# Kernel optimization log

Hardware: AMD Instinct MI355X
Metric: run time of the kernel (lower is better)

The kernel has to match this reference:

```python
import jax, jax.numpy as jnp
import numpy as np

N_NODES = 50000
N_EDGES = 600000
BAG = 16
VOCAB = 10000
EMB = 128
HID = 128
N_CLASSES = 10
N_GRAPHS = 512
PAD_IDX = 1


def setup_inputs() -> dict:
    key = jax.random.key(0)
    ks = jax.random.split(key, 12)
    x_tokens = jax.random.randint(ks[0], (N_NODES, BAG), 0, VOCAB)
    src = jax.random.randint(ks[1], (N_EDGES,), 0, N_NODES)
    dst = jax.random.randint(ks[2], (N_EDGES,), 0, N_NODES)
    edge_index = jnp.stack([src, dst])
    batch = jnp.sort(jax.random.randint(ks[3], (N_NODES,), 0, N_GRAPHS))
    # rows 0,1 are zero in the original (weights[2:] filled from pretrained vectors)
    emb_table = (jax.random.normal(ks[4], (VOCAB, EMB)) * 0.02).at[:2].set(0.0)
    s = 1.0 / np.sqrt(EMB)
    w1_l = jax.random.normal(ks[5], (HID, EMB)) * s
    b1 = jnp.zeros((HID,), jnp.float32)
    w1_r = jax.random.normal(ks[6], (HID, EMB)) * s
    w2_l = jax.random.normal(ks[7], (HID, HID)) * s
    b2 = jnp.zeros((HID,), jnp.float32)
    w2_r = jax.random.normal(ks[8], (HID, HID)) * s
    w_out = jax.random.normal(ks[9], (N_CLASSES, HID)) * s
    b_out = jnp.zeros((N_CLASSES,), jnp.float32)
    return {"x_tokens": x_tokens, "edge_index": edge_index, "batch": batch,
            "emb_table": emb_table, "w1_l": w1_l, "b1": b1, "w1_r": w1_r,
            "w2_l": w2_l, "b2": b2, "w2_r": w2_r, "w_out": w_out, "b_out": b_out}


def _embedding_bag_mean(tokens, table):
    # nn.EmbeddingBag mode='mean' with padding_idx: padding tokens excluded from mean
    emb = table[tokens]                                  # [N, BAG, D]
    mask = (tokens != PAD_IDX)[..., None].astype(table.dtype)
    total = jnp.sum(emb * mask, axis=1)                  # [N, D]
    cnt = jnp.clip(jnp.sum(mask, axis=1), 1.0)           # [N, 1]
    return total / cnt


def _sage_conv(x, src, dst, w_l, b_l, w_r):
    # PyG SAGEConv: lin_l(mean_{j in N(i)} x_j) + lin_r(x_i); lin_r has no bias
    n = x.shape[0]
    msg_sum = jax.ops.segment_sum(x[src], dst, num_segments=n)           # [N, D]
    deg = jax.ops.segment_sum(jnp.ones((src.shape[0], 1), x.dtype), dst,
                              num_segments=n)                             # [N, 1]
    aggr = msg_sum / jnp.clip(deg, 1.0)
    return aggr @ w_l.T + b_l + x @ w_r.T


def reference(x_tokens, edge_index, batch, emb_table, w1_l, b1, w1_r,
              w2_l, b2, w2_r, w_out, b_out):
    src, dst = edge_index[0], edge_index[1]
    x = _embedding_bag_mean(x_tokens, emb_table)                 # [N, EMB]
    x = jax.nn.relu(_sage_conv(x, src, dst, w1_l, b1, w1_r))     # [N, HID]
    x = jax.nn.relu(_sage_conv(x, src, dst, w2_l, b2, w2_r))     # [N, HID]
    # global_mean_pool over graph ids
    g_sum = jax.ops.segment_sum(x, batch, num_segments=N_GRAPHS)
    g_cnt = jax.ops.segment_sum(jnp.ones((x.shape[0], 1), x.dtype), batch,
                                num_segments=N_GRAPHS)
    g = g_sum / jnp.clip(g_cnt, 1.0)                             # [G, HID]
    return g @ w_out.T + b_out                                   # [G, C]
```

## Files before the change

kernel.cpp:

```cpp
#include <hip/hip_runtime.h>
#include <hip/hip_bf16.h>

#define NN 50000
#define NE 600000
#define BAG 16
#define EMB 128
#define HID 128
#define NC 10
#define NG 512
#define PAD_IDX 1
#define VOCAB 10000
#define SLOTS 64
#define TPAIRS (VOCAB * EMB / 2)
#define WPAIRS (4 * HID * EMB / 2)
#define NE8 (NE / 8)
#define SC8BLK ((NE8 + 255) / 256)
#define EMVB (NN / 16)
#define NTILES ((NN + 127) / 128)

typedef __attribute__((ext_vector_type(8))) short v8s;
typedef __attribute__((ext_vector_type(4))) float v4f;

__device__ __forceinline__ float bflo(unsigned u) { return __uint_as_float(u << 16); }
__device__ __forceinline__ float bfhi(unsigned u) { return __uint_as_float(u & 0xffff0000u); }
__device__ __forceinline__ unsigned short f2bf(float f) {
    unsigned u = __float_as_uint(f);
    return (unsigned short)((u + 0x7fffu + ((u >> 16) & 1u)) >> 16);
}
__device__ __forceinline__ void acc8(float* a, v8s v) {
    unsigned* u = (unsigned*)&v;
#pragma unroll
    for (int j = 0; j < 4; j++) {
        a[2 * j] += bflo(u[j]);
        a[2 * j + 1] += bfhi(u[j]);
    }
}

__global__ void k_conv(const float* __restrict__ t, unsigned short* __restrict__ tb,
                       const float* __restrict__ w1l, const float* __restrict__ w1r,
                       const float* __restrict__ w2l, const float* __restrict__ w2r,
                       unsigned short* __restrict__ wbf, int* __restrict__ cnt,
                       float* __restrict__ gsum, float* __restrict__ gcnt) {
    int i = blockIdx.x * blockDim.x + threadIdx.x;
    if (i < NN) cnt[i] = 0;
    if (i < NG * HID) gsum[i] = 0.f;
    if (i < NG) gcnt[i] = 0.f;
    if (i < TPAIRS) {
        float2 v = *(const float2*)(t + (size_t)i * 2);
        unsigned lo = f2bf(v.x), hi = f2bf(v.y);
        *(unsigned*)(tb + (size_t)i * 2) = lo | (hi << 16);
    } else if (i < TPAIRS + WPAIRS) {
        int j = i - TPAIRS;
        int k = j * 2;
        int arr = k >> 14;
        int o = k & 16383;
        const float* w = (arr == 0) ? w1l : (arr == 1) ? w1r : (arr == 2) ? w2l : w2r;
        float2 v = *(const float2*)(w + o);
        unsigned lo = f2bf(v.x), hi = f2bf(v.y);
        *(unsigned*)(wbf + k) = lo | (hi << 16);
    }
}

__global__ __launch_bounds__(256) void k_scatem(const int* __restrict__ src,
                                                const int* __restrict__ dst,
                                                int* __restrict__ cnt,
                                                int* __restrict__ slots,
                                                const int* __restrict__ tokens,
                                                const unsigned short* __restrict__ table,
                                                unsigned short* __restrict__ x0) {
    int b = blockIdx.x;
    if (b < EMVB) {
        int sl = threadIdx.x & 15;
        int node = b * 16 + (threadIdx.x >> 4);
        const int* tp = tokens + node * BAG;
        float a[8];
#pragma unroll
        for (int j = 0; j < 8; j++) a[j] = 0.f;
        int c = 0;
#pragma unroll
        for (int t = 0; t < BAG; t++) {
            int tok = tp[t];
            c += (tok != PAD_IDX);
            v8s v = *(const v8s*)(table + (size_t)tok * EMB + sl * 8);
            acc8(a, v);
        }
        float inv = 1.0f / (float)(c > 0 ? c : 1);
        uint4 o;
        o.x = f2bf(a[0] * inv) | ((unsigned)f2bf(a[1] * inv) << 16);
        o.y = f2bf(a[2] * inv) | ((unsigned)f2bf(a[3] * inv) << 16);
        o.z = f2bf(a[4] * inv) | ((unsigned)f2bf(a[5] * inv) << 16);
        o.w = f2bf(a[6] * inv) | ((unsigned)f2bf(a[7] * inv) << 16);
        *(uint4*)(x0 + (size_t)node * EMB + sl * 8) = o;
        return;
    }
    int t = (b - EMVB) * 256 + threadIdx.x;
    if (t < NE8) {
        int4 s0 = *((const int4*)src + t * 2);
        int4 s1 = *((const int4*)src + t * 2 + 1);
        int4 d0 = *((const int4*)dst + t * 2);
        int4 d1 = *((const int4*)dst + t * 2 + 1);
        int p0 = atomicAdd(&cnt[d0.x], 1);
        int p1 = atomicAdd(&cnt[d0.y], 1);
        int p2 = atomicAdd(&cnt[d0.z], 1);
        int p3 = atomicAdd(&cnt[d0.w], 1);
        int p4 = atomicAdd(&cnt[d1.x], 1);
        int p5 = atomicAdd(&cnt[d1.y], 1);
        int p6 = atomicAdd(&cnt[d1.z], 1);
        int p7 = atomicAdd(&cnt[d1.w], 1);
        if (p0 < SLOTS) slots[(size_t)d0.x * SLOTS + p0] = s0.x;
        if (p1 < SLOTS) slots[(size_t)d0.y * SLOTS + p1] = s0.y;
        if (p2 < SLOTS) slots[(size_t)d0.z * SLOTS + p2] = s0.z;
        if (p3 < SLOTS) slots[(size_t)d0.w * SLOTS + p3] = s0.w;
        if (p4 < SLOTS) slots[(size_t)d1.x * SLOTS + p4] = s1.x;
        if (p5 < SLOTS) slots[(size_t)d1.y * SLOTS + p5] = s1.y;
        if (p6 < SLOTS) slots[(size_t)d1.z * SLOTS + p6] = s1.z;
        if (p7 < SLOTS) slots[(size_t)d1.w * SLOTS + p7] = s1.w;
    }
}

__global__ __launch_bounds__(256) void k_aggr(const unsigned short* __restrict__ x,
                                              const int* __restrict__ cnt,
                                              const int* __restrict__ slots,
                                              unsigned short* __restrict__ aggr) {
    int node = blockIdx.x * 4 + (threadIdx.x >> 6);
    int lane = threadIdx.x & 63;
    if (node >= NN) return;
    int deg = cnt[node];
    int m = deg > SLOTS ? SLOTS : deg;
    int g = lane >> 4, sl = lane & 15;
    float a[8];
#pragma unroll
    for (int j = 0; j < 8; j++) a[j] = 0.f;
    int idx_l = slots[(size_t)node * SLOTS + ((lane < m) ? lane : 0)];
    int i = 0;
    for (; i + 8 <= m; i += 8) {
        int t0 = __shfl(idx_l, i + g, 64);
        int t1 = __shfl(idx_l, i + 4 + g, 64);
        v8s v0 = *(const v8s*)(x + (size_t)t0 * HID + sl * 8);
        v8s v1 = *(const v8s*)(x + (size_t)t1 * HID + sl * 8);
        acc8(a, v0);
        acc8(a, v1);
    }
    for (; i + 4 <= m; i += 4) {
        int t0 = __shfl(idx_l, i + g, 64);
        v8s v0 = *(const v8s*)(x + (size_t)t0 * HID + sl * 8);
        acc8(a, v0);
    }
    int rem = m - i;
    if (rem > 0) {
        int t0 = __shfl(idx_l, (g < rem) ? i + g : i, 64);
        v8s v0 = *(const v8s*)(x + (size_t)t0 * HID + sl * 8);
        if (g < rem) acc8(a, v0);
    }
#pragma unroll
    for (int j = 0; j < 8; j++) {
        a[j] += __shfl_xor(a[j], 16, 64);
        a[j] += __shfl_xor(a[j], 32, 64);
    }
    float inv = 1.0f / (float)(deg > 0 ? deg : 1);
    if (g == 0) {
        uint4 o;
        o.x = f2bf(a[0] * inv) | ((unsigned)f2bf(a[1] * inv) << 16);
        o.y = f2bf(a[2] * inv) | ((unsigned)f2bf(a[3] * inv) << 16);
        o.z = f2bf(a[4] * inv) | ((unsigned)f2bf(a[5] * inv) << 16);
        o.w = f2bf(a[6] * inv) | ((unsigned)f2bf(a[7] * inv) << 16);
        *(uint4*)(aggr + (size_t)node * HID + sl * 8) = o;
    }
}

__device__ __forceinline__ void sage_kloop(int row0, const unsigned short* __restrict__ xa,
                                           const unsigned short* __restrict__ xr,
                                           const unsigned short* __restrict__ wl,
                                           const unsigned short* __restrict__ wr,
                                           unsigned short* As, unsigned short* Bs,
                                           v4f acc[2][8]) {
    int tid = threadIdx.x;
    int wave = tid >> 6, lane = tid & 63;
    int q = lane >> 4, l16 = lane & 15;
    for (int kc = 0; kc < 8; kc++) {
        const unsigned short* Ag = (kc < 4) ? xa : xr;
        const unsigned short* Bg = (kc < 4) ? wl : wr;
        int koff = (kc & 3) * 32;
#pragma unroll
        for (int it = 0; it < 2; it++) {
            int seg = tid + it * 256;
            int r = seg >> 2, sg = seg & 3;
            int gr = row0 + r;
            if (gr > NN - 1) gr = NN - 1;
            v8s a = *(const v8s*)(Ag + (size_t)gr * HID + koff + sg * 8);
            *(v8s*)(As + r * 32 + sg * 8) = a;
            v8s b = *(const v8s*)(Bg + (size_t)r * HID + koff + sg * 8);
            *(v8s*)(Bs + r * 32 + sg * 8) = b;
        }
        __syncthreads();
        v8s a0 = *(const v8s*)(As + (wave * 32 + l16) * 32 + q * 8);
        v8s a1 = *(const v8s*)(As + (wave * 32 + 16 + l16) * 32 + q * 8);
#pragma unroll
        for (int nt = 0; nt < 8; nt++) {
            v8s b = *(const v8s*)(Bs + (nt * 16 + l16) * 32 + q * 8);
            acc[0][nt] = __builtin_amdgcn_mfma_f32_16x16x32_bf16(a0, b, acc[0][nt], 0, 0, 0);
            acc[1][nt] = __builtin_amdgcn_mfma_f32_16x16x32_bf16(a1, b, acc[1][nt], 0, 0, 0);
        }
        __syncthreads();
    }
}

__global__ __launch_bounds__(256) void k_sage(const unsigned short* __restrict__ xa,
                                              const unsigned short* __restrict__ xr,
                                              const unsigned short* __restrict__ wl,
                                              const unsigned short* __restrict__ wr,
                                              const float* __restrict__ bias,
                                              unsigned short* __restrict__ out) {
    __shared__ unsigned short As[128 * 32];
    __shared__ unsigned short Bs[128 * 32];
    int row0 = blockIdx.x * 128;
    v4f acc[2][8];
#pragma unroll
    for (int m = 0; m < 2; m++)
#pragma unroll
        for (int n = 0; n < 8; n++) acc[m][n] = (v4f){0.f, 0.f, 0.f, 0.f};
    sage_kloop(row0, xa, xr, wl, wr, As, Bs, acc);
    int tid = threadIdx.x;
    int wave = tid >> 6, lane = tid & 63;
    int q = lane >> 4, l16 = lane & 15;
#pragma unroll
    for (int nt = 0; nt < 8; nt++) {
        int col = nt * 16 + l16;
        float bv = bias[col];
#pragma unroll
        for (int mt = 0; mt < 2; mt++) {
#pragma unroll
            for (int r = 0; r < 4; r++) {
                int row = row0 + wave * 32 + mt * 16 + q * 4 + r;
                if (row < NN) {
                    float v = acc[mt][nt][r] + bv;
                    v = v > 0.f ? v : 0.f;
                    out[(size_t)row * HID + col] = f2bf(v);
                }
            }
        }
    }
}

__global__ __launch_bounds__(256) void k_sagepool(const unsigned short* __restrict__ xa,
                                                  const unsigned short* __restrict__ xr,
                                                  const unsigned short* __restrict__ wl,
                                                  const unsigned short* __restrict__ wr,
                                                  const float* __restrict__ bias,
                                                  const int* __restrict__ batch,
                                                  float* __restrict__ gsum,
                                                  float* __restrict__ gcnt) {
    __shared__ unsigned short smem[128 * 128];
    unsigned short* As = smem;
    unsigned short* Bs = smem + 128 * 32;
    int row0 = blockIdx.x * 128;
    v4f acc[2][8];
#pragma unroll
    for (int m = 0; m < 2; m++)
#pragma unroll
        for (int n = 0; n < 8; n++) acc[m][n] = (v4f){0.f, 0.f, 0.f, 0.f};
    sage_kloop(row0, xa, xr, wl, wr, As, Bs, acc);
    int tid = threadIdx.x;
    int wave = tid >> 6, lane = tid & 63;
    int q = lane >> 4, l16 = lane & 15;
#pragma unroll
    for (int nt = 0; nt < 8; nt++) {
        int col = nt * 16 + l16;
        float bv = bias[col];
#pragma unroll
        for (int mt = 0; mt < 2; mt++) {
#pragma unroll
            for (int r = 0; r < 4; r++) {
                int rl = wave * 32 + mt * 16 + q * 4 + r;
                float v = acc[mt][nt][r] + bv;
                v = v > 0.f ? v : 0.f;
                smem[rl * 128 + col] = f2bf(v);
            }
        }
    }
    __syncthreads();
    if (tid < 128) {
        int col = tid;
        int end = NN - row0;
        if (end > 128) end = 128;
        int cur = batch[row0];
        float acc_p = 0.f;
        int c = 0;
        for (int i = 0; i < end; i++) {
            int b = batch[row0 + i];
            if (b != cur) {
                atomicAdd(&gsum[cur * HID + col], acc_p);
                if (col == 0) atomicAdd(&gcnt[cur], (float)c);
                acc_p = 0.f;
                c = 0;
                cur = b;
            }
            acc_p += __uint_as_float(((unsigned)smem[i * 128 + col]) << 16);
            c++;
        }
        atomicAdd(&gsum[cur * HID + col], acc_p);
        if (col == 0) atomicAdd(&gcnt[cur], (float)c);
    }
}

__global__ __launch_bounds__(128) void k_final(const float* __restrict__ gsum,
                                               const float* __restrict__ gcnt,
                                               const float* __restrict__ w_out,
                                               const float* __restrict__ b_out,
                                               float* __restrict__ out) {
    __shared__ float mean[HID];
    int g = blockIdx.x, tid = threadIdx.x;
    mean[tid] = gsum[g * HID + tid] / fmaxf(gcnt[g], 1.0f);
    __syncthreads();
    if (tid < NC) {
        float s = b_out[tid];
#pragma unroll 16
        for (int d = 0; d < HID; d++) s += mean[d] * w_out[tid * HID + d];
        out[g * NC + tid] = s;
    }
}

extern "C" void kernel_launch(void* const* d_in, const int* in_sizes, int n_in,
                              void* d_out, int out_size, void* d_ws, size_t ws_size,
                              hipStream_t stream) {
    const int* x_tokens = (const int*)d_in[0];
    const int* edge = (const int*)d_in[1];
    const int* batch = (const int*)d_in[2];
    const float* emb_table = (const float*)d_in[3];
    const float* w1l = (const float*)d_in[4];
    const float* b1 = (const float*)d_in[5];
    const float* w1r = (const float*)d_in[6];
    const float* w2l = (const float*)d_in[7];
    const float* b2 = (const float*)d_in[8];
    const float* w2r = (const float*)d_in[9];
    const float* w_out = (const float*)d_in[10];
    const float* b_out = (const float*)d_in[11];
    float* out = (float*)d_out;

    char* ws = (char*)d_ws;
    size_t off = 0;
    auto alloc = [&](size_t bytes) {
        void* p = ws + off;
        off += (bytes + 255) & ~(size_t)255;
        return p;
    };
    int* cnt = (int*)alloc(NN * 4);
    int* slots = (int*)alloc((size_t)NN * SLOTS * 4);
    unsigned short* wbf = (unsigned short*)alloc(4 * HID * EMB * 2);
    float* gsum = (float*)alloc(NG * HID * 4);
    float* gcnt = (float*)alloc(NG * 4);
    unsigned short* x0 = (unsigned short*)alloc((size_t)NN * EMB * 2);
    unsigned short* x1 = (unsigned short*)alloc((size_t)NN * HID * 2);
    unsigned short* aggrb = (unsigned short*)alloc((size_t)NN * HID * 2);
    unsigned short* table_bf = x1;

    const int* srcp = edge;
    const int* dstp = edge + NE;

    k_conv<<<(TPAIRS + WPAIRS + 255) / 256, 256, 0, stream>>>(
        emb_table, table_bf, w1l, w1r, w2l, w2r, wbf, cnt, gsum, gcnt);
    k_scatem<<<EMVB + SC8BLK, 256, 0, stream>>>(srcp, dstp, cnt, slots, x_tokens,
                                                table_bf, x0);
    k_aggr<<<(NN + 3) / 4, 256, 0, stream>>>(x0, cnt, slots, aggrb);
    k_sage<<<NTILES, 256, 0, stream>>>(aggrb, x0, wbf, wbf + 16384, b1, x1);
    k_aggr<<<(NN + 3) / 4, 256, 0, stream>>>(x1, cnt, slots, aggrb);
    k_sagepool<<<NTILES, 256, 0, stream>>>(aggrb, x1, wbf + 32768, wbf + 49152, b2,
                                           batch, gsum, gcnt);
    k_final<<<NG, 128, 0, stream>>>(gsum, gcnt, w_out, b_out, out);
}
```

Measured before the change: 211.2 us.

## Interleave per-edge scatter with embedding-bag work in the same threads

```diff
diff --git a/kernel.cpp b/kernel.cpp
--- a/kernel.cpp
+++ b/kernel.cpp
@@ -13,8 +13,6 @@
 #define SLOTS 64
 #define TPAIRS (VOCAB * EMB / 2)
 #define WPAIRS (4 * HID * EMB / 2)
-#define NE8 (NE / 8)
-#define SC8BLK ((NE8 + 255) / 256)
 #define EMVB (NN / 16)
 #define NTILES ((NN + 127) / 128)
 
@@ -69,53 +67,49 @@
                                                 const unsigned short* __restrict__ table,
                                                 unsigned short* __restrict__ x0) {
     int b = blockIdx.x;
-    if (b < EMVB) {
-        int sl = threadIdx.x & 15;
-        int node = b * 16 + (threadIdx.x >> 4);
-        const int* tp = tokens + node * BAG;
-        float a[8];
-#pragma unroll
-        for (int j = 0; j < 8; j++) a[j] = 0.f;
-        int c = 0;
-#pragma unroll
-        for (int t = 0; t < BAG; t++) {
-            int tok = tp[t];
-            c += (tok != PAD_IDX);
-            v8s v = *(const v8s*)(table + (size_t)tok * EMB + sl * 8);
-            acc8(a, v);
-        }
-        float inv = 1.0f / (float)(c > 0 ? c : 1);
-        uint4 o;
-        o.x = f2bf(a[0] * inv) | ((unsigned)f2bf(a[1] * inv) << 16);
-        o.y = f2bf(a[2] * inv) | ((unsigned)f2bf(a[3] * inv) << 16);
-        o.z = f2bf(a[4] * inv) | ((unsigned)f2bf(a[5] * inv) << 16);
-        o.w = f2bf(a[6] * inv) | ((unsigned)f2bf(a[7] * inv) << 16);
-        *(uint4*)(x0 + (size_t)node * EMB + sl * 8) = o;
-        return;
-    }
-    int t = (b - EMVB) * 256 + threadIdx.x;
-    if (t < NE8) {
-        int4 s0 = *((const int4*)src + t * 2);
-        int4 s1 = *((const int4*)src + t * 2 + 1);
-        int4 d0 = *((const int4*)dst + t * 2);
-        int4 d1 = *((const int4*)dst + t * 2 + 1);
-        int p0 = atomicAdd(&cnt[d0.x], 1);
-        int p1 = atomicAdd(&cnt[d0.y], 1);
-        int p2 = atomicAdd(&cnt[d0.z], 1);
-        int p3 = atomicAdd(&cnt[d0.w], 1);
-        int p4 = atomicAdd(&cnt[d1.x], 1);
-        int p5 = atomicAdd(&cnt[d1.y], 1);
-        int p6 = atomicAdd(&cnt[d1.z], 1);
-        int p7 = atomicAdd(&cnt[d1.w], 1);
-        if (p0 < SLOTS) slots[(size_t)d0.x * SLOTS + p0] = s0.x;
-        if (p1 < SLOTS) slots[(size_t)d0.y * SLOTS + p1] = s0.y;
-        if (p2 < SLOTS) slots[(size_t)d0.z * SLOTS + p2] = s0.z;
-        if (p3 < SLOTS) slots[(size_t)d0.w * SLOTS + p3] = s0.w;
-        if (p4 < SLOTS) slots[(size_t)d1.x * SLOTS + p4] = s1.x;
-        if (p5 < SLOTS) slots[(size_t)d1.y * SLOTS + p5] = s1.y;
-        if (p6 < SLOTS) slots[(size_t)d1.z * SLOTS + p6] = s1.z;
-        if (p7 < SLOTS) slots[(size_t)d1.w * SLOTS + p7] = s1.w;
-    }
+    int tid = threadIdx.x;
+
+    int e = b * 256 + tid;
+    int s_src = 0, s_dst = 0, p = SLOTS;
+    bool has_e = (e < NE);
+    if (has_e) {
+        s_src = src[e];
+        s_dst = dst[e];
+        p = atomicAdd(&cnt[s_dst], 1);
+    }
+
+    int sl = tid & 15;
+    int node = b * 16 + (tid >> 4);
+    const int* tp = tokens + node * BAG;
+    int tk[16];
+    *(int4*)(tk) = *(const int4*)(tp);
+    *(int4*)(tk + 4) = *(const int4*)(tp + 4);
+    *(int4*)(tk + 8) = *(const int4*)(tp + 8);
+    *(int4*)(tk + 12) = *(const int4*)(tp + 12);
+    int c = 0;
+#pragma unroll
+    for (int t = 0; t < BAG; t++) c += (tk[t] != PAD_IDX);
+    float a[8];
+#pragma unroll
+    for (int j = 0; j < 8; j++) a[j] = 0.f;
+#pragma unroll
+    for (int h = 0; h < 2; h++) {
+        v8s v[8];
+#pragma unroll
+        for (int t = 0; t < 8; t++)
+            v[t] = *(const v8s*)(table + (size_t)tk[h * 8 + t] * EMB + sl * 8);
+#pragma unroll
+        for (int t = 0; t < 8; t++) acc8(a, v[t]);
+    }
+    float inv = 1.0f / (float)(c > 0 ? c : 1);
+    uint4 o;
+    o.x = f2bf(a[0] * inv) | ((unsigned)f2bf(a[1] * inv) << 16);
+    o.y = f2bf(a[2] * inv) | ((unsigned)f2bf(a[3] * inv) << 16);
+    o.z = f2bf(a[4] * inv) | ((unsigned)f2bf(a[5] * inv) << 16);
+    o.w = f2bf(a[6] * inv) | ((unsigned)f2bf(a[7] * inv) << 16);
+    *(uint4*)(x0 + (size_t)node * EMB + sl * 8) = o;
+
+    if (has_e && p < SLOTS) slots[(size_t)s_dst * SLOTS + p] = s_src;
 }
 
 __global__ __launch_bounds__(256) void k_aggr(const unsigned short* __restrict__ x,
@@ -359,8 +353,8 @@
 
     k_conv<<<(TPAIRS + WPAIRS + 255) / 256, 256, 0, stream>>>(
         emb_table, table_bf, w1l, w1r, w2l, w2r, wbf, cnt, gsum, gcnt);
-    k_scatem<<<EMVB + SC8BLK, 256, 0, stream>>>(srcp, dstp, cnt, slots, x_tokens,
-                                                table_bf, x0);
+    k_scatem<<<EMVB, 256, 0, stream>>>(srcp, dstp, cnt, slots, x_tokens,
+                                       table_bf, x0);
     k_aggr<<<(NN + 3) / 4, 256, 0, stream>>>(x0, cnt, slots, aggrb);
     k_sage<<<NTILES, 256, 0, stream>>>(aggrb, x0, wbf, wbf + 16384, b1, x1);
     k_aggr<<<(NN + 3) / 4, 256, 0, stream>>>(x1, cnt, slots, aggrb);
```

Result: faster. 205.9 us (-2.5%).
